# Optimization experiments

Measured on AMD Instinct MI355X. Metric: run time of the kernel, lower is better.

The kernel has to match this reference:

```python
import jax, jax.numpy as jnp
import numpy as np

N_NODES = 50000

def _sage_mean(x, src, tgt, Wl, bl, Wr):
    # PyG SAGEConv(aggr='mean'): out = lin_l(mean_{j in N(i)} x_j) + lin_r(x_i)
    # aggregate in input dim first (cheaper), then transform
    agg = jax.ops.segment_sum(x[src], tgt, num_segments=N_NODES)  # [N, Din]
    deg = jax.ops.segment_sum(jnp.ones((src.shape[0],), x.dtype), tgt, num_segments=N_NODES)
    mean = agg / jnp.maximum(deg, 1.0)[:, None]
    return mean @ Wl + bl + x @ Wr

def setup_inputs() -> dict:
    key = jax.random.key(0)
    ks = jax.random.split(key, 16)
    d_in, d0, d1 = 64, 256, 128  # input, initial_channels=2*128, hidden
    d_out = 8
    s = 0.02
    x = jax.random.normal(ks[0], (N_NODES, d_in), dtype=jnp.float32)
    edge_index = jax.random.randint(ks[1], (2, 800000), 0, N_NODES, dtype=jnp.int64)
    p = lambda k, sh: s * jax.random.normal(k, sh, dtype=jnp.float32)
    return {
        "x": x, "edge_index": edge_index,
        # first_conv: 64 -> 256
        "Wf_l": p(ks[2], (d_in, d0)), "bf": jnp.zeros((d0,), jnp.float32), "Wf_r": p(ks[3], (d_in, d0)),
        # conv0: 256 -> 128
        "W0_l": p(ks[4], (d0, d1)), "b0": jnp.zeros((d1,), jnp.float32), "W0_r": p(ks[5], (d0, d1)),
        # conv1: 128 -> 128
        "W1_l": p(ks[6], (d1, d1)), "b1": jnp.zeros((d1,), jnp.float32), "W1_r": p(ks[7], (d1, d1)),
        # head MLP
        "W_lin": p(ks[8], (d1, d1)), "b_lin": jnp.zeros((d1,), jnp.float32),
        "W_lin2": p(ks[9], (d1, d_out)), "b_lin2": jnp.zeros((d_out,), jnp.float32),
    }

def reference(x, edge_index, Wf_l, bf, Wf_r, W0_l, b0, W0_r, W1_l, b1, W1_r, W_lin, b_lin, W_lin2, b_lin2):
    src, tgt = edge_index[0], edge_index[1]
    h = jax.nn.relu(_sage_mean(x, src, tgt, Wf_l, bf, Wf_r))
    h = jax.nn.relu(_sage_mean(h, src, tgt, W0_l, b0, W0_r))
    h = jax.nn.relu(_sage_mean(h, src, tgt, W1_l, b1, W1_r))
    h = h @ W_lin + b_lin
    return h @ W_lin2 + b_lin2
```

## Files before the change

### kernel.cpp

```cpp
#include <hip/hip_runtime.h>
#include <hip/hip_fp16.h>


typedef __attribute__((ext_vector_type(8))) short bf16x8;
typedef __attribute__((ext_vector_type(4))) float f32x4;

struct Seg { const unsigned short* A; const unsigned short* W; int lda; int ldw; int K; };
struct Segs { Seg s[4]; int n; };

__device__ __forceinline__ unsigned short f2bf(float x) {
  unsigned u = __float_as_uint(x);
  u += 0x7FFF + ((u >> 16) & 1);
  return (unsigned short)(u >> 16);
}
__device__ __forceinline__ unsigned short f2h(float x) {
  return __half_as_ushort(__float2half(x));
}
__device__ __forceinline__ float2 ld_h2(const unsigned short* p, size_t idx) {
  unsigned uv = *(const unsigned*)(p + idx);
  __half2 h = *reinterpret_cast<__half2*>(&uv);
  return __half22float2(h);
}


__global__ __launch_bounds__(256) void hist_k(const int* __restrict__ tgt, int* __restrict__ histT,
                                              int E, int NB, int CH) {
  extern __shared__ int sh[];
  int g = blockIdx.x, tid = threadIdx.x;
  for (int b = tid; b < NB; b += 256) sh[b] = 0;
  __syncthreads();
  int eb = g * CH, ee = min(eb + CH, E);
  for (int i = eb + tid; i < ee; i += 256)
    atomicAdd(&sh[tgt[i] >> 6], 1);
  __syncthreads();
  for (int b = tid; b < NB; b += 256) histT[b * 64 + g] = sh[b];
}

__global__ __launch_bounds__(256) void scanb_k(int* __restrict__ histT, int* __restrict__ bcnt, int NB) {
  int wv = threadIdx.x >> 6, lane = threadIdx.x & 63;
  int b = blockIdx.x * 4 + wv;
  if (b >= NB) return;
  int v = histT[b * 64 + lane];
  int x = v;
#pragma unroll
  for (int o = 1; o < 64; o <<= 1) {
    int y = __shfl_up(x, o);
    if (lane >= o) x += y;
  }
  histT[b * 64 + lane] = x - v;
  if (lane == 63) bcnt[b] = x;
}

__global__ __launch_bounds__(1024) void bscan_k(const int* __restrict__ bcnt, int* __restrict__ boff,
                                                int* __restrict__ row_ptr, int NB, int E, int N) {
  __shared__ int sh[1024];
  int tid = threadIdx.x;
  int v = (tid < NB) ? bcnt[tid] : 0;
  int val = v;
  sh[tid] = val;
  __syncthreads();
  for (int o = 1; o < 1024; o <<= 1) {
    int t = (tid >= o) ? sh[tid - o] : 0;
    __syncthreads();
    val += t;
    sh[tid] = val;
    __syncthreads();
  }
  if (tid < NB) boff[tid] = val - v;
  if (tid == NB - 1) boff[NB] = val;
  if (tid == 0) row_ptr[N] = E;
}

__global__ __launch_bounds__(256) void scatter_k(const int* __restrict__ src, const int* __restrict__ tgt,
                                                 const int* __restrict__ boff, const int* __restrict__ histT,
                                                 unsigned* __restrict__ vals, int E, int NB, int CH) {
  extern __shared__ int sh[];
  int g = blockIdx.x, tid = threadIdx.x;
  for (int b = tid; b < NB; b += 256) sh[b] = boff[b] + histT[b * 64 + g];
  __syncthreads();
  int eb = g * CH, ee = min(eb + CH, E);
  for (int i = eb + tid; i < ee; i += 256) {
    int t = tgt[i], s = src[i];
    int pos = atomicAdd(&sh[t >> 6], 1);
    vals[pos] = (unsigned)s | ((unsigned)(t & 63) << 17);
  }
}

__global__ __launch_bounds__(256) void bsort_k(const unsigned* __restrict__ vals, const int* __restrict__ boff,
                                               int* __restrict__ row_ptr, int* __restrict__ srcs, int N) {
  int b = blockIdx.x;
  int base = b << 6;
  int s0 = boff[b], s1 = boff[b + 1];
  __shared__ int hist[64], excl[64], cur[64];
  int tid = threadIdx.x;
  if (tid < 64) { hist[tid] = 0; cur[tid] = 0; }
  __syncthreads();
  for (int i = s0 + tid; i < s1; i += 256)
    atomicAdd(&hist[(vals[i] >> 17) & 63], 1);
  __syncthreads();
  if (tid < 64) {
    int v = hist[tid];
    int x = v;
#pragma unroll
    for (int o = 1; o < 64; o <<= 1) {
      int y = __shfl_up(x, o);
      if (tid >= o) x += y;
    }
    excl[tid] = x - v;
    int node = base + tid;
    if (node < N) row_ptr[node] = s0 + x - v;
  }
  __syncthreads();
  for (int i = s0 + tid; i < s1; i += 256) {
    unsigned v = vals[i];
    int l = (v >> 17) & 63;
    int pos = s0 + excl[l] + atomicAdd(&cur[l], 1);
    srcs[pos] = (int)(v & 0x1FFFF);
  }
}

__device__ __forceinline__ void split_store(float v, unsigned short* hi, unsigned short* lo, int idx) {
  unsigned short h = f2bf(v);
  float hf = __uint_as_float(((unsigned)h) << 16);
  hi[idx] = h;
  lo[idx] = f2bf(v - hf);
}

__global__ __launch_bounds__(256) void prep_k(
    const float* __restrict__ x, unsigned short* __restrict__ xb, unsigned short* __restrict__ xh, int nbConv, int n4,
    const float* __restrict__ Wf_l, const float* __restrict__ Wf_r,
    unsigned short* __restrict__ Wt1hi, unsigned short* __restrict__ Wt1lo,
    const float* __restrict__ W0_l, const float* __restrict__ W0_r, unsigned short* __restrict__ Wt2hi,
    const float* __restrict__ W1_l, const float* __restrict__ W1_r, unsigned short* __restrict__ Wt3hi,
    const float* __restrict__ Wlin, const float* __restrict__ blin,
    const float* __restrict__ Wlin2, const float* __restrict__ blin2,
    float* __restrict__ Wc, float* __restrict__ bc) {
  int b = blockIdx.x, t = threadIdx.x;
  if (b < nbConv) {
    int i = b * 256 + t;
    if (i < n4) {
      float4 v = ((const float4*)x)[i];
      ((ushort2*)xb)[i * 2]     = make_ushort2(f2bf(v.x), f2bf(v.y));
      ((ushort2*)xb)[i * 2 + 1] = make_ushort2(f2bf(v.z), f2bf(v.w));
      ((ushort2*)xh)[i * 2]     = make_ushort2(f2h(v.x), f2h(v.y));
      ((ushort2*)xh)[i * 2 + 1] = make_ushort2(f2h(v.z), f2h(v.w));
    }
    return;
  }
  b -= nbConv;
  if (b < 128) {
    int idx = b * 256 + t;
    int n = idx >> 7, k = idx & 127;
    float v = (k < 64) ? Wf_l[k * 256 + n] : Wf_r[(k - 64) * 256 + n];
    split_store(v, Wt1hi, Wt1lo, idx);
    return;
  }
  b -= 128;
  if (b < 256) {
    int idx = b * 256 + t;
    int n = idx >> 8, k = idx & 255;
    float v = (n < 128) ? W0_l[k * 128 + n] : W0_r[k * 128 + (n - 128)];
    Wt2hi[idx] = f2bf(v);
    return;
  }
  b -= 256;
  if (b < 128) {
    int idx = b * 256 + t;
    int n = idx >> 7, k = idx & 127;
    float v = (n < 128) ? W1_l[k * 128 + n] : W1_r[k * 128 + (n - 128)];
    Wt3hi[idx] = f2bf(v);
    return;
  }
  b -= 128;
  {
    int idx = b * 256 + t;
    if (idx < 1024) {
      int i = idx >> 3, j = idx & 7;
      float acc = 0.f;
      for (int k = 0; k < 128; ++k) acc = fmaf(Wlin[i * 128 + k], Wlin2[k * 8 + j], acc);
      Wc[idx] = acc;
    }
    if (idx < 8) {
      float acc = blin2[idx];
      for (int k = 0; k < 128; ++k) acc = fmaf(blin[k], Wlin2[k * 8 + idx], acc);
      bc[idx] = acc;
    }
  }
}

__global__ __launch_bounds__(256) void agg_mean64_k(const unsigned short* __restrict__ xh, const int* __restrict__ rp,
                                                    const int* __restrict__ srcs, unsigned short* __restrict__ mb, int n) {
  int w = threadIdx.x >> 6, lane = threadIdx.x & 63;
  int node = blockIdx.x * 4 + w;
  if (node >= n) return;
  int s0 = rp[node], s1 = rp[node + 1];
  float sum = 0.f;
  int e = s0;
  for (; e + 7 < s1; e += 8) {
    int i0 = srcs[e], i1 = srcs[e + 1], i2 = srcs[e + 2], i3 = srcs[e + 3];
    int i4 = srcs[e + 4], i5 = srcs[e + 5], i6 = srcs[e + 6], i7 = srcs[e + 7];
    float v0 = __half2float(__ushort_as_half(xh[(size_t)i0 * 64 + lane]));
    float v1 = __half2float(__ushort_as_half(xh[(size_t)i1 * 64 + lane]));
    float v2 = __half2float(__ushort_as_half(xh[(size_t)i2 * 64 + lane]));
    float v3 = __half2float(__ushort_as_half(xh[(size_t)i3 * 64 + lane]));
    float v4 = __half2float(__ushort_as_half(xh[(size_t)i4 * 64 + lane]));
    float v5 = __half2float(__ushort_as_half(xh[(size_t)i5 * 64 + lane]));
    float v6 = __half2float(__ushort_as_half(xh[(size_t)i6 * 64 + lane]));
    float v7 = __half2float(__ushort_as_half(xh[(size_t)i7 * 64 + lane]));
    sum += ((v0 + v1) + (v2 + v3)) + ((v4 + v5) + (v6 + v7));
  }
  for (; e < s1; ++e)
    sum += __half2float(__ushort_as_half(xh[(size_t)srcs[e] * 64 + lane]));
  int deg = s1 - s0;
  float inv = 1.f / (float)(deg > 0 ? deg : 1);
  mb[(size_t)node * 64 + lane] = f2bf(sum * inv);
}

template <int OUTMODE>
__global__ __launch_bounds__(256) void agg128_k(const unsigned short* __restrict__ yb,
                                                const unsigned short* __restrict__ zb,
                                                const float* __restrict__ bias,
                                                const int* __restrict__ rp, const int* __restrict__ srcs,
                                                void* __restrict__ hout,
                                                const float* __restrict__ Wc, const float* __restrict__ bc, int n) {
  int w = threadIdx.x >> 6, lane = threadIdx.x & 63;
  int node = blockIdx.x * 4 + w;
  if (node >= n) return;
  int s0 = rp[node], s1 = rp[node + 1];
  int d = lane * 2;
  float sx = 0.f, sy = 0.f;
  int e = s0;
  for (; e + 7 < s1; e += 8) {
    int i0 = srcs[e], i1 = srcs[e + 1], i2 = srcs[e + 2], i3 = srcs[e + 3];
    int i4 = srcs[e + 4], i5 = srcs[e + 5], i6 = srcs[e + 6], i7 = srcs[e + 7];
    float2 v0 = ld_h2(yb, (size_t)i0 * 128 + d);
    float2 v1 = ld_h2(yb, (size_t)i1 * 128 + d);
    float2 v2 = ld_h2(yb, (size_t)i2 * 128 + d);
    float2 v3 = ld_h2(yb, (size_t)i3 * 128 + d);
    float2 v4 = ld_h2(yb, (size_t)i4 * 128 + d);
    float2 v5 = ld_h2(yb, (size_t)i5 * 128 + d);
    float2 v6 = ld_h2(yb, (size_t)i6 * 128 + d);
    float2 v7 = ld_h2(yb, (size_t)i7 * 128 + d);
    sx += ((v0.x + v1.x) + (v2.x + v3.x)) + ((v4.x + v5.x) + (v6.x + v7.x));
    sy += ((v0.y + v1.y) + (v2.y + v3.y)) + ((v4.y + v5.y) + (v6.y + v7.y));
  }
  for (; e < s1; ++e) {
    float2 v = ld_h2(yb, (size_t)srcs[e] * 128 + d);
    sx += v.x; sy += v.y;
  }
  int deg = s1 - s0;
  float inv = 1.f / (float)(deg > 0 ? deg : 1);
  float2 z = ld_h2(zb, (size_t)node * 128 + d);
  float2 b2 = *(const float2*)&bias[d];
  float ox = fmaxf(fmaf(sx, inv, z.x + b2.x), 0.f);
  float oy = fmaxf(fmaf(sy, inv, z.y + b2.y), 0.f);

  if (OUTMODE == 1) {
    ((ushort2*)hout)[((size_t)node * 128 + d) / 2] = make_ushort2(f2bf(ox), f2bf(oy));
  } else {
    const float4* wr = (const float4*)&Wc[d * 8];
    float4 wa0 = wr[0], wa1 = wr[1], wb0 = wr[2], wb1 = wr[3];
    float a8[8];
    a8[0] = ox * wa0.x + oy * wb0.x;
    a8[1] = ox * wa0.y + oy * wb0.y;
    a8[2] = ox * wa0.z + oy * wb0.z;
    a8[3] = ox * wa0.w + oy * wb0.w;
    a8[4] = ox * wa1.x + oy * wb1.x;
    a8[5] = ox * wa1.y + oy * wb1.y;
    a8[6] = ox * wa1.z + oy * wb1.z;
    a8[7] = ox * wa1.w + oy * wb1.w;
#pragma unroll
    for (int off = 32; off >= 1; off >>= 1) {
#pragma unroll
      for (int j = 0; j < 8; ++j) a8[j] += __shfl_xor(a8[j], off);
    }
    if (lane == 0) {
      float* o = (float*)hout + (size_t)node * 8;
      *(float4*)o       = make_float4(a8[0] + bc[0], a8[1] + bc[1], a8[2] + bc[2], a8[3] + bc[3]);
      *(float4*)(o + 4) = make_float4(a8[4] + bc[4], a8[5] + bc[5], a8[6] + bc[6], a8[7] + bc[7]);
    }
  }
}

template <int MODE>
__global__ __launch_bounds__(256) void gemm_mfma_k(Segs segs, const float* __restrict__ bias,
                                                   unsigned short* __restrict__ Y, unsigned short* __restrict__ Z,
                                                   unsigned short* __restrict__ Ob, int ldc) {
  __shared__ unsigned short Asl[128 * 32];
  __shared__ unsigned short Wsl[128 * 32];
  int tid = threadIdx.x;
  int lane = tid & 63, wave = tid >> 6;
  int wm = wave & 1, wn = wave >> 1;
  int rowBase = blockIdx.x * 128, colBase = blockIdx.y * 128;
  f32x4 acc[4][4] = {};

  int c0 = tid, c1 = tid + 256;
  int r0 = c0 >> 2, q0 = c0 & 3;
  int r1 = c1 >> 2, q1 = c1 & 3;
  int ml = lane & 15, qq = lane >> 4;

  for (int si = 0; si < segs.n; ++si) {
    const unsigned short* Aseg = segs.s[si].A;
    const unsigned short* Wseg = segs.s[si].W;
    int lda = segs.s[si].lda, ldw = segs.s[si].ldw, K = segs.s[si].K;
    for (int k0 = 0; k0 < K; k0 += 32) {
      uint4 av0 = *(const uint4*)&Aseg[(size_t)(rowBase + r0) * lda + k0 + q0 * 8];
      uint4 av1 = *(const uint4*)&Aseg[(size_t)(rowBase + r1) * lda + k0 + q1 * 8];
      uint4 wv0 = *(const uint4*)&Wseg[(size_t)(colBase + r0) * ldw + k0 + q0 * 8];
      uint4 wv1 = *(const uint4*)&Wseg[(size_t)(colBase + r1) * ldw + k0 + q1 * 8];
      __syncthreads();
      *(uint4*)&Asl[c0 * 8] = av0;
      *(uint4*)&Asl[c1 * 8] = av1;
      *(uint4*)&Wsl[c0 * 8] = wv0;
      *(uint4*)&Wsl[c1 * 8] = wv1;
      __syncthreads();
      bf16x8 af[4], bw[4];
#pragma unroll
      for (int i = 0; i < 4; ++i) {
        af[i] = *(bf16x8*)&Asl[(wm * 64 + i * 16 + ml) * 32 + qq * 8];
        bw[i] = *(bf16x8*)&Wsl[(wn * 64 + i * 16 + ml) * 32 + qq * 8];
      }
#pragma unroll
      for (int mf = 0; mf < 4; ++mf)
#pragma unroll
        for (int nf = 0; nf < 4; ++nf)
          acc[mf][nf] = __builtin_amdgcn_mfma_f32_16x16x32_bf16(af[mf], bw[nf], acc[mf][nf], 0, 0, 0);
    }
  }

  if (MODE == 0) {
    unsigned short* dst = (colBase == 0) ? Y : Z;
#pragma unroll
    for (int mf = 0; mf < 4; ++mf) {
      int row = rowBase + wm * 64 + mf * 16 + qq * 4;
#pragma unroll
      for (int nf = 0; nf < 4; ++nf) {
        int col = wn * 64 + nf * 16 + ml;
#pragma unroll
        for (int r = 0; r < 4; ++r)
          dst[(size_t)(row + r) * 128 + col] = f2h(acc[mf][nf][r]);
      }
    }
  } else {
    float bc4[4];
#pragma unroll
    for (int nf = 0; nf < 4; ++nf) bc4[nf] = bias[colBase + wn * 64 + nf * 16 + ml];
#pragma unroll
    for (int mf = 0; mf < 4; ++mf) {
      int row = rowBase + wm * 64 + mf * 16 + qq * 4;
#pragma unroll
      for (int nf = 0; nf < 4; ++nf) {
        int col = colBase + wn * 64 + nf * 16 + ml;
#pragma unroll
        for (int r = 0; r < 4; ++r) {
          float o = fmaxf(acc[mf][nf][r] + bc4[nf], 0.f);
          Ob[(size_t)(row + r) * ldc + col] = f2bf(o);
        }
      }
    }
  }
}

extern "C" void kernel_launch(void* const* d_in, const int* in_sizes, int n_in,
                              void* d_out, int out_size, void* d_ws, size_t ws_size,
                              hipStream_t stream) {
  const float* x      = (const float*)d_in[0];
  const int*   ei     = (const int*)d_in[1];
  const float* Wf_l   = (const float*)d_in[2];
  const float* bf     = (const float*)d_in[3];
  const float* Wf_r   = (const float*)d_in[4];
  const float* W0_l   = (const float*)d_in[5];
  const float* b0     = (const float*)d_in[6];
  const float* W0_r   = (const float*)d_in[7];
  const float* W1_l   = (const float*)d_in[8];
  const float* b1     = (const float*)d_in[9];
  const float* W1_r   = (const float*)d_in[10];
  const float* W_lin  = (const float*)d_in[11];
  const float* b_lin  = (const float*)d_in[12];
  const float* W_lin2 = (const float*)d_in[13];
  const float* b_lin2 = (const float*)d_in[14];
  float* out = (float*)d_out;

  const int N = in_sizes[0] / 64;
  const int E = in_sizes[1] / 2;
  const int Npad = ((N + 127) / 128) * 128;
  const int nblkM = Npad / 128;
  const int NB = (N + 63) / 64;
  const int G  = 64;
  const int CH = (E + G - 1) / G;
  const int* e_src = ei;
  const int* e_tgt = ei + E;

  size_t off = 0;
  char* base = (char*)d_ws;
  auto carve = [&](size_t bytes) -> void* {
    void* p = base + off;
    off += (bytes + 255) & ~(size_t)255;
    return p;
  };
  int*      row_ptr = (int*)carve((size_t)(N + 1) * 4);
  int*      bcnt    = (int*)carve((size_t)NB * 4);
  int*      boff    = (int*)carve((size_t)(NB + 1) * 4);
  int*      histT   = (int*)carve((size_t)NB * G * 4);
  unsigned* vals    = (unsigned*)carve((size_t)E * 4);
  int*      srcs    = (int*)carve((size_t)E * 4);
  unsigned short* xb    = (unsigned short*)carve((size_t)Npad * 64 * 2);
  unsigned short* xh    = (unsigned short*)carve((size_t)Npad * 64 * 2);
  unsigned short* mb    = (unsigned short*)carve((size_t)Npad * 64 * 2);
  unsigned short* h1b   = (unsigned short*)carve((size_t)Npad * 256 * 2);
  unsigned short* h2b   = (unsigned short*)carve((size_t)Npad * 128 * 2);
  unsigned short* yb    = (unsigned short*)carve((size_t)Npad * 128 * 2);
  unsigned short* zb    = (unsigned short*)carve((size_t)Npad * 128 * 2);
  unsigned short* Wt1hi = (unsigned short*)carve(256 * 128 * 2);
  unsigned short* Wt1lo = (unsigned short*)carve(256 * 128 * 2);
  unsigned short* Wt2hi = (unsigned short*)carve(256 * 256 * 2);
  unsigned short* Wt3hi = (unsigned short*)carve(256 * 128 * 2);
  float* Wcomb = (float*)carve(1024 * 4);
  float* bcomb = (float*)carve(8 * 4);
  (void)ws_size; (void)n_in; (void)out_size;

  const int nbConv = (N * 16 + 255) / 256;
  const size_t ldsNB = (size_t)NB * 4;

  hist_k<<<G, 256, ldsNB, stream>>>(e_tgt, histT, E, NB, CH);
  scanb_k<<<(NB + 3) / 4, 256, 0, stream>>>(histT, bcnt, NB);
  bscan_k<<<1, 1024, 0, stream>>>(bcnt, boff, row_ptr, NB, E, N);
  scatter_k<<<G, 256, ldsNB, stream>>>(e_src, e_tgt, boff, histT, vals, E, NB, CH);
  bsort_k<<<NB, 256, 0, stream>>>(vals, boff, row_ptr, srcs, N);

  prep_k<<<nbConv + 128 + 256 + 128 + 4, 256, 0, stream>>>(
      x, xb, xh, nbConv, N * 16,
      Wf_l, Wf_r, Wt1hi, Wt1lo,
      W0_l, W0_r, Wt2hi,
      W1_l, W1_r, Wt3hi,
      W_lin, b_lin, W_lin2, b_lin2, Wcomb, bcomb);

  const int nbAgg = (N + 3) / 4;
  const dim3 gemmGrid(nblkM, 2);

  agg_mean64_k<<<nbAgg, 256, 0, stream>>>(xh, row_ptr, srcs, mb, N);
  {
    Segs s;
    s.n = 4;
    s.s[0] = {mb, Wt1hi,      64, 128, 64};
    s.s[1] = {xb, Wt1hi + 64, 64, 128, 64};
    s.s[2] = {mb, Wt1lo,      64, 128, 64};
    s.s[3] = {xb, Wt1lo + 64, 64, 128, 64};
    gemm_mfma_k<1><<<gemmGrid, 256, 0, stream>>>(s, bf, nullptr, nullptr, h1b, 256);
  }

  {
    Segs s;
    s.n = 1;
    s.s[0] = {h1b, Wt2hi, 256, 256, 256};
    s.s[1] = {nullptr, nullptr, 0, 0, 0};
    s.s[2] = {nullptr, nullptr, 0, 0, 0};
    s.s[3] = {nullptr, nullptr, 0, 0, 0};
    gemm_mfma_k<0><<<gemmGrid, 256, 0, stream>>>(s, nullptr, yb, zb, nullptr, 256);
  }
  agg128_k<1><<<nbAgg, 256, 0, stream>>>(yb, zb, b0, row_ptr, srcs, h2b, nullptr, nullptr, N);

  {
    Segs s;
    s.n = 1;
    s.s[0] = {h2b, Wt3hi, 128, 128, 128};
    s.s[1] = {nullptr, nullptr, 0, 0, 0};
    s.s[2] = {nullptr, nullptr, 0, 0, 0};
    s.s[3] = {nullptr, nullptr, 0, 0, 0};
    gemm_mfma_k<0><<<gemmGrid, 256, 0, stream>>>(s, nullptr, yb, zb, nullptr, 256);
  }
  agg128_k<2><<<nbAgg, 256, 0, stream>>>(yb, zb, b1, row_ptr, srcs, out, Wcomb, bcomb, N);
}
```

Baseline: 315.6 us.

## Vectorize gather aggregation with 16-byte loads and lane groups per edge

```diff
diff --git a/kernel.cpp b/kernel.cpp
--- a/kernel.cpp
+++ b/kernel.cpp
@@ -16,12 +16,15 @@
 __device__ __forceinline__ unsigned short f2h(float x) {
   return __half_as_ushort(__float2half(x));
 }
-__device__ __forceinline__ float2 ld_h2(const unsigned short* p, size_t idx) {
-  unsigned uv = *(const unsigned*)(p + idx);
-  __half2 h = *reinterpret_cast<__half2*>(&uv);
+__device__ __forceinline__ float2 h2f(unsigned u) {
+  __half2 h = *reinterpret_cast<__half2*>(&u);
   return __half22float2(h);
 }
-
+__device__ __forceinline__ void acc8(float* acc, uint4 v) {
+  float2 a = h2f(v.x), b = h2f(v.y), c = h2f(v.z), d = h2f(v.w);
+  acc[0] += a.x; acc[1] += a.y; acc[2] += b.x; acc[3] += b.y;
+  acc[4] += c.x; acc[5] += c.y; acc[6] += d.x; acc[7] += d.y;
+}
 
 __global__ __launch_bounds__(256) void hist_k(const int* __restrict__ tgt, int* __restrict__ histT,
                                               int E, int NB, int CH) {
@@ -193,27 +196,42 @@
   int w = threadIdx.x >> 6, lane = threadIdx.x & 63;
   int node = blockIdx.x * 4 + w;
   if (node >= n) return;
+  int grp = lane >> 3, sl = lane & 7;
+  int d0 = sl * 8;
   int s0 = rp[node], s1 = rp[node + 1];
-  float sum = 0.f;
+  float acc[8] = {0.f, 0.f, 0.f, 0.f, 0.f, 0.f, 0.f, 0.f};
   int e = s0;
-  for (; e + 7 < s1; e += 8) {
-    int i0 = srcs[e], i1 = srcs[e + 1], i2 = srcs[e + 2], i3 = srcs[e + 3];
-    int i4 = srcs[e + 4], i5 = srcs[e + 5], i6 = srcs[e + 6], i7 = srcs[e + 7];
-    float v0 = __half2float(__ushort_as_half(xh[(size_t)i0 * 64 + lane]));
-    float v1 = __half2float(__ushort_as_half(xh[(size_t)i1 * 64 + lane]));
-    float v2 = __half2float(__ushort_as_half(xh[(size_t)i2 * 64 + lane]));
-    float v3 = __half2float(__ushort_as_half(xh[(size_t)i3 * 64 + lane]));
-    float v4 = __half2float(__ushort_as_half(xh[(size_t)i4 * 64 + lane]));
-    float v5 = __half2float(__ushort_as_half(xh[(size_t)i5 * 64 + lane]));
-    float v6 = __half2float(__ushort_as_half(xh[(size_t)i6 * 64 + lane]));
-    float v7 = __half2float(__ushort_as_half(xh[(size_t)i7 * 64 + lane]));
-    sum += ((v0 + v1) + (v2 + v3)) + ((v4 + v5) + (v6 + v7));
-  }
-  for (; e < s1; ++e)
-    sum += __half2float(__ushort_as_half(xh[(size_t)srcs[e] * 64 + lane]));
+  for (; e + 16 <= s1; e += 16) {
+    int ia = srcs[e + grp];
+    int ib = srcs[e + 8 + grp];
+    uint4 va = *(const uint4*)&xh[(size_t)ia * 64 + d0];
+    uint4 vb = *(const uint4*)&xh[(size_t)ib * 64 + d0];
+    acc8(acc, va);
+    acc8(acc, vb);
+  }
+  for (; e < s1; e += 8) {
+    int idx = e + grp;
+    if (idx < s1) {
+      int ia = srcs[idx];
+      uint4 va = *(const uint4*)&xh[(size_t)ia * 64 + d0];
+      acc8(acc, va);
+    }
+  }
+#pragma unroll
+  for (int j = 0; j < 8; ++j) {
+    acc[j] += __shfl_xor(acc[j], 8);
+    acc[j] += __shfl_xor(acc[j], 16);
+    acc[j] += __shfl_xor(acc[j], 32);
+  }
   int deg = s1 - s0;
   float inv = 1.f / (float)(deg > 0 ? deg : 1);
-  mb[(size_t)node * 64 + lane] = f2bf(sum * inv);
+  if (grp == 0) {
+    unsigned p0 = (unsigned)f2bf(acc[0] * inv) | ((unsigned)f2bf(acc[1] * inv) << 16);
+    unsigned p1 = (unsigned)f2bf(acc[2] * inv) | ((unsigned)f2bf(acc[3] * inv) << 16);
+    unsigned p2 = (unsigned)f2bf(acc[4] * inv) | ((unsigned)f2bf(acc[5] * inv) << 16);
+    unsigned p3 = (unsigned)f2bf(acc[6] * inv) | ((unsigned)f2bf(acc[7] * inv) << 16);
+    *(uint4*)&mb[(size_t)node * 64 + d0] = make_uint4(p0, p1, p2, p3);
+  }
 }
 
 template <int OUTMODE>
@@ -226,58 +244,73 @@
   int w = threadIdx.x >> 6, lane = threadIdx.x & 63;
   int node = blockIdx.x * 4 + w;
   if (node >= n) return;
+  int grp = lane >> 4, sl = lane & 15;
+  int d0 = sl * 8;
   int s0 = rp[node], s1 = rp[node + 1];
-  int d = lane * 2;
-  float sx = 0.f, sy = 0.f;
+  float acc[8] = {0.f, 0.f, 0.f, 0.f, 0.f, 0.f, 0.f, 0.f};
   int e = s0;
-  for (; e + 7 < s1; e += 8) {
-    int i0 = srcs[e], i1 = srcs[e + 1], i2 = srcs[e + 2], i3 = srcs[e + 3];
-    int i4 = srcs[e + 4], i5 = srcs[e + 5], i6 = srcs[e + 6], i7 = srcs[e + 7];
-    float2 v0 = ld_h2(yb, (size_t)i0 * 128 + d);
-    float2 v1 = ld_h2(yb, (size_t)i1 * 128 + d);
-    float2 v2 = ld_h2(yb, (size_t)i2 * 128 + d);
-    float2 v3 = ld_h2(yb, (size_t)i3 * 128 + d);
-    float2 v4 = ld_h2(yb, (size_t)i4 * 128 + d);
-    float2 v5 = ld_h2(yb, (size_t)i5 * 128 + d);
-    float2 v6 = ld_h2(yb, (size_t)i6 * 128 + d);
-    float2 v7 = ld_h2(yb, (size_t)i7 * 128 + d);
-    sx += ((v0.x + v1.x) + (v2.x + v3.x)) + ((v4.x + v5.x) + (v6.x + v7.x));
-    sy += ((v0.y + v1.y) + (v2.y + v3.y)) + ((v4.y + v5.y) + (v6.y + v7.y));
-  }
-  for (; e < s1; ++e) {
-    float2 v = ld_h2(yb, (size_t)srcs[e] * 128 + d);
-    sx += v.x; sy += v.y;
+  for (; e + 8 <= s1; e += 8) {
+    int ia = srcs[e + grp];
+    int ib = srcs[e + 4 + grp];
+    uint4 va = *(const uint4*)&yb[(size_t)ia * 128 + d0];
+    uint4 vb = *(const uint4*)&yb[(size_t)ib * 128 + d0];
+    acc8(acc, va);
+    acc8(acc, vb);
+  }
+  for (; e < s1; e += 4) {
+    int idx = e + grp;
+    if (idx < s1) {
+      int ia = srcs[idx];
+      uint4 va = *(const uint4*)&yb[(size_t)ia * 128 + d0];
+      acc8(acc, va);
+    }
+  }
+#pragma unroll
+  for (int j = 0; j < 8; ++j) {
+    acc[j] += __shfl_xor(acc[j], 16);
+    acc[j] += __shfl_xor(acc[j], 32);
   }
   int deg = s1 - s0;
   float inv = 1.f / (float)(deg > 0 ? deg : 1);
-  float2 z = ld_h2(zb, (size_t)node * 128 + d);
-  float2 b2 = *(const float2*)&bias[d];
-  float ox = fmaxf(fmaf(sx, inv, z.x + b2.x), 0.f);
-  float oy = fmaxf(fmaf(sy, inv, z.y + b2.y), 0.f);
+  uint4 zv = *(const uint4*)&zb[(size_t)node * 128 + d0];
+  float2 za = h2f(zv.x), zc = h2f(zv.y), zd = h2f(zv.z), ze = h2f(zv.w);
+  float zf[8] = {za.x, za.y, zc.x, zc.y, zd.x, zd.y, ze.x, ze.y};
+  float4 b0v = *(const float4*)&bias[d0];
+  float4 b1v = *(const float4*)&bias[d0 + 4];
+  float bf8[8] = {b0v.x, b0v.y, b0v.z, b0v.w, b1v.x, b1v.y, b1v.z, b1v.w};
+  float o[8];
+#pragma unroll
+  for (int j = 0; j < 8; ++j)
+    o[j] = fmaxf(fmaf(acc[j], inv, zf[j] + bf8[j]), 0.f);
 
   if (OUTMODE == 1) {
-    ((ushort2*)hout)[((size_t)node * 128 + d) / 2] = make_ushort2(f2bf(ox), f2bf(oy));
+    if (grp == 0) {
+      unsigned p0 = (unsigned)f2bf(o[0]) | ((unsigned)f2bf(o[1]) << 16);
+      unsigned p1 = (unsigned)f2bf(o[2]) | ((unsigned)f2bf(o[3]) << 16);
+      unsigned p2 = (unsigned)f2bf(o[4]) | ((unsigned)f2bf(o[5]) << 16);
+      unsigned p3 = (unsigned)f2bf(o[6]) | ((unsigned)f2bf(o[7]) << 16);
+      *(uint4*)&((unsigned short*)hout)[(size_t)node * 128 + d0] = make_uint4(p0, p1, p2, p3);
+    }
   } else {
-    const float4* wr = (const float4*)&Wc[d * 8];
-    float4 wa0 = wr[0], wa1 = wr[1], wb0 = wr[2], wb1 = wr[3];
-    float a8[8];
-    a8[0] = ox * wa0.x + oy * wb0.x;
-    a8[1] = ox * wa0.y + oy * wb0.y;
-    a8[2] = ox * wa0.z + oy * wb0.z;
-    a8[3] = ox * wa0.w + oy * wb0.w;
-    a8[4] = ox * wa1.x + oy * wb1.x;
-    a8[5] = ox * wa1.y + oy * wb1.y;
-    a8[6] = ox * wa1.z + oy * wb1.z;
-    a8[7] = ox * wa1.w + oy * wb1.w;
-#pragma unroll
-    for (int off = 32; off >= 1; off >>= 1) {
+    float a8[8] = {0.f, 0.f, 0.f, 0.f, 0.f, 0.f, 0.f, 0.f};
+#pragma unroll
+    for (int j = 0; j < 8; ++j) {
+      const float4* wr = (const float4*)&Wc[(d0 + j) * 8];
+      float4 w0 = wr[0], w1 = wr[1];
+      a8[0] = fmaf(o[j], w0.x, a8[0]); a8[1] = fmaf(o[j], w0.y, a8[1]);
+      a8[2] = fmaf(o[j], w0.z, a8[2]); a8[3] = fmaf(o[j], w0.w, a8[3]);
+      a8[4] = fmaf(o[j], w1.x, a8[4]); a8[5] = fmaf(o[j], w1.y, a8[5]);
+      a8[6] = fmaf(o[j], w1.z, a8[6]); a8[7] = fmaf(o[j], w1.w, a8[7]);
+    }
+#pragma unroll
+    for (int off = 1; off <= 8; off <<= 1) {
 #pragma unroll
       for (int j = 0; j < 8; ++j) a8[j] += __shfl_xor(a8[j], off);
     }
     if (lane == 0) {
-      float* o = (float*)hout + (size_t)node * 8;
-      *(float4*)o       = make_float4(a8[0] + bc[0], a8[1] + bc[1], a8[2] + bc[2], a8[3] + bc[3]);
-      *(float4*)(o + 4) = make_float4(a8[4] + bc[4], a8[5] + bc[5], a8[6] + bc[6], a8[7] + bc[7]);
+      float* op = (float*)hout + (size_t)node * 8;
+      *(float4*)op       = make_float4(a8[0] + bc[0], a8[1] + bc[1], a8[2] + bc[2], a8[3] + bc[3]);
+      *(float4*)(op + 4) = make_float4(a8[4] + bc[4], a8[5] + bc[5], a8[6] + bc[6], a8[7] + bc[7]);
     }
   }
 }
```

After: 358.3 us. 13.5% more time.
